# Optimization experiments

Measured on AMD Instinct MI355X. Metric: run time of the kernel, lower is better.

## Reference

```python
import jax, jax.numpy as jnp
import numpy as np

B, S, E, H = 4, 2048, 1024, 4
D = E // H  # head_dim = 256


def setup_inputs() -> dict:
    key = jax.random.key(0)
    ks = jax.random.split(key, 9)
    scale = 1.0 / np.sqrt(E)
    return {
        "hidden_states": jax.random.normal(ks[0], (B, S, E), jnp.float32),
        "Wq": jax.random.normal(ks[1], (E, E), jnp.float32) * scale,
        "Wk": jax.random.normal(ks[2], (E, E), jnp.float32) * scale,
        "Wv": jax.random.normal(ks[3], (E, E), jnp.float32) * scale,
        "Wo": jax.random.normal(ks[4], (E, E), jnp.float32) * scale,
        "bo": jax.random.normal(ks[5], (E,), jnp.float32) * 0.02,
        "betas": jax.random.normal(ks[6], (1, H, 1, 1), jnp.float32),
        "mem": jax.random.uniform(ks[7], (H, D, D), jnp.float32),
        "z": jax.random.uniform(ks[8], (H, D, 1), jnp.float32),
    }


def _split_heads(t):  # [B,S,E] -> [B,H,S,D]
    return t.reshape(B, S, H, D).transpose(0, 2, 1, 3)


def reference(hidden_states, Wq, Wk, Wv, Wo, bo, betas, mem, z):
    q = _split_heads(hidden_states @ Wq)  # [B,H,S,D]
    k = _split_heads(hidden_states @ Wk)
    v = _split_heads(hidden_states @ Wv)

    # linear-attention feature map (ELU + 1)
    sigma_q = jax.nn.elu(q) + 1.0
    sigma_k = jax.nn.elu(k) + 1.0

    # compressive-memory read: mem [H,D,D], z [H,D,1] broadcast over batch
    A_mem = (sigma_q @ mem) / (sigma_q @ z + 1e-6)  # [B,H,S,D]

    # standard causal softmax attention
    attn_weights = jnp.einsum("bhqd,bhkd->bhqk", q, k)
    causal = jnp.tril(jnp.ones((S, S), bool))
    mask_value = jnp.finfo(attn_weights.dtype).min
    attn_weights = jnp.where(causal, attn_weights, mask_value)
    attn_weights = jax.nn.softmax(attn_weights, axis=-1)
    attn_output = jnp.einsum("bhqk,bhkd->bhqd", attn_weights, v)

    # per-head sigmoid gate mixing memory read and local attention
    gate = jax.nn.sigmoid(betas)  # [1,H,1,1]
    attn_output = gate * A_mem + (1.0 - gate) * attn_output

    # memory update (delta rule)
    delta = (sigma_k @ mem) / (sigma_k @ z + 1e-6)  # [B,H,S,D]
    mem_new = mem + jnp.einsum("bhsd,bhse->bhde", sigma_k, v - delta)  # [B,H,D,D]
    z_new = z + sigma_k.sum(axis=-2, keepdims=True).transpose(0, 1, 3, 2)  # [B,H,D,1]

    out = attn_output.transpose(0, 2, 1, 3).reshape(B, S, E) @ Wo + bo
    return out, mem_new, z_new
```

## Files before the change

### kernel.cpp

```cpp
#include <hip/hip_runtime.h>
#include <math.h>

#define Bn 4
#define Sn 2048
#define En 1024
#define Hn 4
#define Dn 256

typedef _Float16 half8 __attribute__((ext_vector_type(8)));
typedef _Float16 half4v __attribute__((ext_vector_type(4)));
typedef float floatx4 __attribute__((ext_vector_type(4)));

#define MFMA16(a, b, c) __builtin_amdgcn_mfma_f32_16x16x32_f16((a), (b), (c), 0, 0, 0)

__device__ __forceinline__ float elup1(float x) {
    return x > 0.0f ? x + 1.0f : __expf(x);
}

__global__ void cvt_h_k(const float* __restrict__ src, _Float16* __restrict__ dst, int n4) {
    int idx = blockIdx.x * 256 + threadIdx.x;
    const int stride = gridDim.x * 256;
    for (; idx < n4; idx += stride) {
        float4 v = ((const float4*)src)[idx];
        half4v o;
        o[0] = (_Float16)v.x; o[1] = (_Float16)v.y;
        o[2] = (_Float16)v.z; o[3] = (_Float16)v.w;
        ((half4v*)dst)[idx] = o;
    }
}

__global__ __launch_bounds__(256) void trans_f32f16_k(
    const float* __restrict__ src, _Float16* __restrict__ dst, int R, int C) {
    __shared__ float T[64][65];
    const int tid = threadIdx.x;
    const int c0 = blockIdx.x * 64, r0 = blockIdx.y * 64;
    src += (size_t)blockIdx.z * R * C;
    dst += (size_t)blockIdx.z * R * C;
    {
        const int tr = tid >> 2, tc = (tid & 3) * 16;
        const float* s = src + (size_t)(r0 + tr) * C + c0 + tc;
        #pragma unroll
        for (int i = 0; i < 4; ++i) {
            float4 v = *(const float4*)(s + i * 4);
            T[tr][tc + i * 4 + 0] = v.x;
            T[tr][tc + i * 4 + 1] = v.y;
            T[tr][tc + i * 4 + 2] = v.z;
            T[tr][tc + i * 4 + 3] = v.w;
        }
    }
    __syncthreads();
    {
        const int cr = tid >> 2, rc = (tid & 3) * 16;
        half8 h0, h1;
        #pragma unroll
        for (int i = 0; i < 8; ++i) h0[i] = (_Float16)T[rc + i][cr];
        #pragma unroll
        for (int i = 0; i < 8; ++i) h1[i] = (_Float16)T[rc + 8 + i][cr];
        _Float16* d = dst + (size_t)(c0 + cr) * R + r0 + rc;
        *(half8*)d = h0;
        *(half8*)(d + 8) = h1;
    }
}

__global__ __launch_bounds__(256) void trans_h16_k(
    const _Float16* __restrict__ Vh, _Float16* __restrict__ Vtg) {
    __shared__ __align__(16) unsigned short T[64 * 72];
    const int tid = threadIdx.x;
    const int s0 = blockIdx.x * 64;
    const int e0 = blockIdx.y * 64;
    const int b = blockIdx.z;
    const int h = e0 >> 8, d0 = e0 & 255;
    {
        const int tr = tid >> 2, tc = (tid & 3) * 16;
        const _Float16* s = Vh + (size_t)(b * Sn + s0 + tr) * En + e0 + tc;
        _Float16* d = (_Float16*)T + tr * 72 + tc;
        *(half8*)d = *(const half8*)s;
        *(half8*)(d + 8) = *(const half8*)(s + 8);
    }
    __syncthreads();
    {
        const int dr = tid >> 2, sc = (tid & 3) * 16;
        const _Float16* Tp = (const _Float16*)T;
        half8 h0, h1;
        #pragma unroll
        for (int i = 0; i < 8; ++i) h0[i] = Tp[(sc + i) * 72 + dr];
        #pragma unroll
        for (int i = 0; i < 8; ++i) h1[i] = Tp[(sc + 8 + i) * 72 + dr];
        _Float16* d = Vtg + (size_t)((b * 4 + h) * 256 + d0 + dr) * (size_t)Sn + s0 + sc;
        *(half8*)d = h0;
        *(half8*)(d + 8) = h1;
    }
}

template <bool OUT32>
__global__ __launch_bounds__(256) void gemm_fused_k(
    const _Float16* __restrict__ A, const _Float16* __restrict__ Bt,
    _Float16* __restrict__ Qo, _Float16* __restrict__ Ko, _Float16* __restrict__ Vo,
    float* __restrict__ C32, const float* __restrict__ bias) {
    __shared__ __align__(16) unsigned short Ah[128 * 72];
    __shared__ __align__(16) unsigned short Bh[128 * 72];
    const int tid = threadIdx.x;
    const int lane = tid & 63, w = tid >> 6, quad = lane >> 4, l15 = lane & 15;
    const int bm = blockIdx.y * 128, bn = blockIdx.x * 128;
    const int wr = (w >> 1) * 64, wc = (w & 1) * 64;
    floatx4 acc[4][4];
    #pragma unroll
    for (int mt = 0; mt < 4; ++mt)
        #pragma unroll
        for (int nt = 0; nt < 4; ++nt) acc[mt][nt] = (floatx4){0.f, 0.f, 0.f, 0.f};

    const int srow = tid >> 1, skoff = (tid & 1) * 32;
    const _Float16* as = A + (size_t)(bm + srow) * 1024 + skoff;
    const _Float16* bs = Bt + (size_t)(bn + srow) * 1024 + skoff;
    _Float16* ad = (_Float16*)Ah + srow * 72 + skoff;
    _Float16* bd = (_Float16*)Bh + srow * 72 + skoff;
    const _Float16* AhF = (const _Float16*)Ah;
    const _Float16* BhF = (const _Float16*)Bh;

    for (int k0 = 0; k0 < 1024; k0 += 64) {
        if (k0) __syncthreads();
        #pragma unroll
        for (int u = 0; u < 4; ++u) {
            *(half8*)(ad + u * 8) = *(const half8*)(as + k0 + u * 8);
            *(half8*)(bd + u * 8) = *(const half8*)(bs + k0 + u * 8);
        }
        __syncthreads();
        #pragma unroll
        for (int ks = 0; ks < 2; ++ks) {
            half8 af[4], bf[4];
            #pragma unroll
            for (int mt = 0; mt < 4; ++mt)
                af[mt] = *(const half8*)(AhF + (wr + mt * 16 + l15) * 72 + ks * 32 + quad * 8);
            #pragma unroll
            for (int nt = 0; nt < 4; ++nt)
                bf[nt] = *(const half8*)(BhF + (wc + nt * 16 + l15) * 72 + ks * 32 + quad * 8);
            #pragma unroll
            for (int mt = 0; mt < 4; ++mt)
                #pragma unroll
                for (int nt = 0; nt < 4; ++nt)
                    acc[mt][nt] = MFMA16(af[mt], bf[nt], acc[mt][nt]);
        }
    }
    #pragma unroll
    for (int mt = 0; mt < 4; ++mt)
        #pragma unroll
        for (int nt = 0; nt < 4; ++nt)
            #pragma unroll
            for (int r = 0; r < 4; ++r) {
                const int row = bm + wr + mt * 16 + quad * 4 + r;
                const int col = bn + wc + nt * 16 + l15;
                if constexpr (OUT32) {
                    C32[(size_t)row * 1024 + col] = acc[mt][nt][r] + bias[col];
                } else {
                    const int m = col >> 10, c = col & 1023;
                    _Float16* dst = (m == 0) ? Qo : ((m == 1) ? Ko : Vo);
                    dst[(size_t)row * 1024 + c] = (_Float16)acc[mt][nt][r];
                }
            }
}

__global__ __launch_bounds__(256, 3) void flash_gate_k(
    const _Float16* __restrict__ Qh, const _Float16* __restrict__ Khg,
    const _Float16* __restrict__ Vtg, const _Float16* __restrict__ memT,
    const float* __restrict__ zp, const float* __restrict__ betas,
    _Float16* __restrict__ Cmb, _Float16* __restrict__ Opart,
    float* __restrict__ mpart, float* __restrict__ lpart) {
    __shared__ __align__(16) unsigned short Pb[4 * 16 * 40];
    const int tid = threadIdx.x;
    const int lane = tid & 63;
    const int w = tid >> 6, quad = lane >> 4, l15 = lane & 15;
    const int bx = blockIdx.x, bh = blockIdx.y;
    const int b = bh >> 2, h = bh & 3;

    int qt, kt0, kt1, unit;
    if (bx < 32) {
        qt = 31 - (bx >> 1);
        unit = bx & 1;
        kt0 = unit ? (qt + 1) : 0;
        kt1 = unit ? (2 * qt + 2) : (qt + 1);
    } else {
        qt = 15 - (bx - 32);
        unit = 0;
        kt0 = 0;
        kt1 = 2 * qt + 2;
    }
    const bool two = (bx < 32);
    const int q0 = qt * 64;

    const _Float16* Qrow = Qh + (size_t)(b * Sn + q0 + w * 16 + l15) * En + h * Dn;
    half8 qf[8];
    #pragma unroll
    for (int kc = 0; kc < 8; ++kc) qf[kc] = *(const half8*)(Qrow + kc * 32 + quad * 8);

    floatx4 acc[17];
    #pragma unroll
    for (int nt = 0; nt < 17; ++nt) acc[nt] = (floatx4){0.f, 0.f, 0.f, 0.f};
    half8 ones;
    #pragma unroll
    for (int j = 0; j < 8; ++j) ones[j] = (_Float16)1.0f;

    const float gate = 1.0f / (1.0f + __expf(-betas[h]));
    const float omg = 1.0f - gate;
    _Float16* Cb = Cmb + (size_t)(b * Sn + q0 + w * 16) * En + h * Dn;
    _Float16* PbF = (_Float16*)Pb;

    if (unit == 0) {
        float denp = 0.0f;
        const _Float16* memh = memT + (size_t)h * Dn * Dn + (size_t)l15 * Dn + quad * 8;
        for (int dc = 0; dc < 8; ++dc) {
            half8 sv;
            const float* zb = zp + h * Dn + dc * 32 + quad * 8;
            #pragma unroll
            for (int j = 0; j < 8; ++j) {
                const float s = elup1((float)qf[dc][j]);
                sv[j] = (_Float16)s;
                denp += s * zb[j];
            }
            #pragma unroll
            for (int nt = 0; nt < 16; ++nt) {
                half8 bmf = *(const half8*)(memh + (size_t)(nt * 16) * Dn + dc * 32);
                acc[nt] = MFMA16(sv, bmf, acc[nt]);
            }
        }
        denp += __shfl_xor(denp, 16);
        denp += __shfl_xor(denp, 32);
        const float deninv = 1.0f / (denp + 1e-6f);
        float den4[4];
        #pragma unroll
        for (int r = 0; r < 4; ++r) den4[r] = __shfl(deninv, quad * 4 + r);
        #pragma unroll
        for (int nt = 0; nt < 16; ++nt)
            #pragma unroll
            for (int r = 0; r < 4; ++r) {
                Cb[(size_t)(quad * 4 + r) * En + nt * 16 + l15] =
                    (_Float16)(gate * acc[nt][r] * den4[r]);
                acc[nt][r] = 0.0f;
            }
    }

    const _Float16* kb0 = Khg + (size_t)(b * Sn + kt0 * 32 + l15) * En + h * Dn + quad * 8;
    const _Float16* kb1 = kb0 + (size_t)16 * En;
    const _Float16* vb = Vtg + (size_t)(bh * 256 + l15) * Sn + kt0 * 32 + quad * 8;
    float mold[4] = {-1e30f, -1e30f, -1e30f, -1e30f};

    for (int kt = kt0; kt < kt1; ++kt) {
        floatx4 S0 = (floatx4){0.f, 0.f, 0.f, 0.f};
        floatx4 S1 = (floatx4){0.f, 0.f, 0.f, 0.f};
        #pragma unroll
        for (int kc = 0; kc < 8; ++kc) {
            half8 kf0 = *(const half8*)(kb0 + kc * 32);
            half8 kf1 = *(const half8*)(kb1 + kc * 32);
            S0 = MFMA16(qf[kc], kf0, S0);
            S1 = MFMA16(qf[kc], kf1, S1);
        }
        kb0 += (size_t)32 * En;
        kb1 += (size_t)32 * En;
        if (kt >= 2 * qt) {
            const int k0 = kt * 32;
            #pragma unroll
            for (int r = 0; r < 4; ++r) {
                const int qg = q0 + w * 16 + quad * 4 + r;
                if (k0 + l15 > qg) S0[r] = -1e30f;
                if (k0 + 16 + l15 > qg) S1[r] = -1e30f;
            }
        }
        float alpha[4];
        bool nr = true;
        #pragma unroll
        for (int r = 0; r < 4; ++r) {
            float mx = fmaxf(S0[r], S1[r]);
            mx = fmaxf(mx, __shfl_xor(mx, 1));
            mx = fmaxf(mx, __shfl_xor(mx, 2));
            mx = fmaxf(mx, __shfl_xor(mx, 4));
            mx = fmaxf(mx, __shfl_xor(mx, 8));
            const float mnew = fmaxf(mold[r], mx);
            alpha[r] = __expf(mold[r] - mnew);
            nr = nr && (mnew == mold[r]);
            mold[r] = mnew;
            const float p0 = __expf(S0[r] - mnew);
            const float p1 = __expf(S1[r] - mnew);
            _Float16* pr = PbF + (w * 16 + quad * 4 + r) * 40;
            pr[l15] = (_Float16)p0;
            pr[16 + l15] = (_Float16)p1;
        }
        if (__ballot(nr) != 0xFFFFFFFFFFFFFFFFull) {
            #pragma unroll
            for (int nt = 0; nt < 17; ++nt) {
                acc[nt][0] *= alpha[0];
                acc[nt][1] *= alpha[1];
                acc[nt][2] *= alpha[2];
                acc[nt][3] *= alpha[3];
            }
        }
        __asm__ volatile("s_waitcnt lgkmcnt(0)" ::: "memory");
        half8 pf = *(const half8*)(PbF + (w * 16 + l15) * 40 + quad * 8);
        #pragma unroll
        for (int nt = 0; nt < 16; ++nt) {
            half8 vf = *(const half8*)(vb + (size_t)(nt * 16) * Sn);
            acc[nt] = MFMA16(pf, vf, acc[nt]);
        }
        acc[16] = MFMA16(pf, ones, acc[16]);
        vb += 32;
    }

    if (!two) {
        #pragma unroll
        for (int r = 0; r < 4; ++r) {
            const float sc = omg / acc[16][r];
            #pragma unroll
            for (int nt = 0; nt < 16; ++nt) {
                const size_t idx = (size_t)(quad * 4 + r) * En + nt * 16 + l15;
                Cb[idx] = (_Float16)((float)Cb[idx] + acc[nt][r] * sc);
            }
        }
    } else {
        const int pidx = ((qt - 16) * 16 + bh) * 2 + unit;
        _Float16* Op = Opart + ((size_t)pidx * 64 + w * 16) * 256;
        #pragma unroll
        for (int nt = 0; nt < 16; ++nt)
            #pragma unroll
            for (int r = 0; r < 4; ++r)
                Op[(quad * 4 + r) * 256 + nt * 16 + l15] = (_Float16)acc[nt][r];
        if (l15 == 0) {
            #pragma unroll
            for (int r = 0; r < 4; ++r) {
                mpart[pidx * 64 + w * 16 + quad * 4 + r] = mold[r];
                lpart[pidx * 64 + w * 16 + quad * 4 + r] = acc[16][r];
            }
        }
    }
}

__global__ __launch_bounds__(256) void merge_k(
    const _Float16* __restrict__ Opart, const float* __restrict__ mpart,
    const float* __restrict__ lpart, const float* __restrict__ betas,
    _Float16* __restrict__ Cmb) {
    const int qi = blockIdx.x;
    const int bh = blockIdx.y;
    const int b = bh >> 2, h = bh & 3;
    const int tid = threadIdx.x;
    const int idx = (qi * 16 + bh) * 2;
    const float gate = 1.0f / (1.0f + __expf(-betas[h]));
    const float omg = 1.0f - gate;
    const int rsub = tid >> 6;
    const int c0 = (tid & 63) * 4;
    const _Float16* O0 = Opart + (size_t)idx * 64 * 256;
    const _Float16* O1 = O0 + 64 * 256;
    const int q0 = (16 + qi) * 64;
    for (int chunk = 0; chunk < 16; ++chunk) {
        const int r = chunk * 4 + rsub;
        const float m0 = mpart[idx * 64 + r], l0 = lpart[idx * 64 + r];
        const float m1 = mpart[(idx + 1) * 64 + r], l1 = lpart[(idx + 1) * 64 + r];
        const float mm = fmaxf(m0, m1);
        const float s0 = __expf(m0 - mm), s1 = __expf(m1 - mm);
        const float rl = omg / (l0 * s0 + l1 * s1);
        half4v o0 = *(const half4v*)(O0 + r * 256 + c0);
        half4v o1 = *(const half4v*)(O1 + r * 256 + c0);
        _Float16* cp = Cmb + (size_t)(b * Sn + q0 + r) * En + h * Dn + c0;
        half4v cv = *(half4v*)cp;
        #pragma unroll
        for (int j = 0; j < 4; ++j)
            cv[j] = (_Float16)((float)cv[j] + ((float)o0[j] * s0 + (float)o1[j] * s1) * rl);
        *(half4v*)cp = cv;
    }
}

__global__ __launch_bounds__(256) void delta_ut_k(
    const _Float16* __restrict__ Kg, _Float16* __restrict__ Vtg,
    _Float16* __restrict__ SkT, const _Float16* __restrict__ memT,
    const float* __restrict__ zp) {
    __shared__ __align__(16) unsigned short L[256 * 72];
    const int tid = threadIdx.x;
    const int lane = tid & 63;
    const int w = tid >> 6, quad = lane >> 4, l15 = lane & 15;
    const int s0 = blockIdx.x * 64;
    const int bh = blockIdx.y;
    const int b = bh >> 2, h = bh & 3;
    _Float16* Lf = (_Float16*)L;

    const _Float16* Krow = Kg + (size_t)(b * Sn + s0 + w * 16 + l15) * En + h * Dn;
    half8 skf[8];
    float denp = 0.0f;
    #pragma unroll
    for (int kc = 0; kc < 8; ++kc) {
        half8 kv = *(const half8*)(Krow + kc * 32 + quad * 8);
        const float* zb = zp + h * Dn + kc * 32 + quad * 8;
        #pragma unroll
        for (int j = 0; j < 8; ++j) {
            const float s = elup1((float)kv[j]);
            skf[kc][j] = (_Float16)s;
            denp += s * zb[j];
        }
    }
    denp += __shfl_xor(denp, 16);
    denp += __shfl_xor(denp, 32);
    const float deninv = 1.0f / (denp + 1e-6f);
    float den4[4];
    #pragma unroll
    for (int r = 0; r < 4; ++r) den4[r] = __shfl(deninv, quad * 4 + r);

    floatx4 acc[16];
    #pragma unroll
    for (int nt = 0; nt < 16; ++nt) acc[nt] = (floatx4){0.f, 0.f, 0.f, 0.f};
    const _Float16* memh = memT + (size_t)h * Dn * Dn + (size_t)l15 * Dn + quad * 8;
    #pragma unroll
    for (int kc = 0; kc < 8; ++kc)
        #pragma unroll
        for (int nt = 0; nt < 16; ++nt) {
            half8 bmf = *(const half8*)(memh + (size_t)(nt * 16) * Dn + kc * 32);
            acc[nt] = MFMA16(skf[kc], bmf, acc[nt]);
        }

    #pragma unroll
    for (int nt = 0; nt < 16; ++nt)
        #pragma unroll
        for (int r = 0; r < 4; ++r)
            Lf[(nt * 16 + l15) * 72 + w * 16 + quad * 4 + r] =
                (_Float16)(acc[nt][r] * den4[r]);
    __syncthreads();
    {
        _Float16* Vrow = Vtg + (size_t)(bh * 256 + tid) * Sn + s0;
        #pragma unroll
        for (int u = 0; u < 8; ++u) {
            half8 v = *(const half8*)(Vrow + u * 8);
            half8 d = *(const half8*)(Lf + tid * 72 + u * 8);
            #pragma unroll
            for (int j = 0; j < 8; ++j) v[j] = v[j] - d[j];
            *(half8*)(Vrow + u * 8) = v;
        }
    }
    __syncthreads();
    #pragma unroll
    for (int kc = 0; kc < 8; ++kc)
        #pragma unroll
        for (int j = 0; j < 8; ++j)
            Lf[(kc * 32 + quad * 8 + j) * 72 + w * 16 + l15] = skf[kc][j];
    __syncthreads();
    {
        _Float16* Srow = SkT + (size_t)(bh * 256 + tid) * Sn + s0;
        #pragma unroll
        for (int u = 0; u < 8; ++u)
            *(half8*)(Srow + u * 8) = *(const half8*)(Lf + tid * 72 + u * 8);
    }
}

__global__ __launch_bounds__(256) void memupd_k(
    const _Float16* __restrict__ SkT, const _Float16* __restrict__ UT,
    const float* __restrict__ memp, float* __restrict__ mem_new) {
    __shared__ __align__(16) unsigned short Ah[64 * 72];
    __shared__ __align__(16) unsigned short Bh[64 * 72];
    const int tid = threadIdx.x;
    const int lane = tid & 63, w = tid >> 6, quad = lane >> 4, l15 = lane & 15;
    const int bn = blockIdx.x * 64, bm = blockIdx.y * 64;
    const int bh = blockIdx.z, h = bh & 3;
    const _Float16* Ab = SkT + (size_t)(bh * 256 + bm) * Sn;
    const _Float16* Bb = UT + (size_t)(bh * 256 + bn) * Sn;
    floatx4 acc[4];
    #pragma unroll
    for (int nt = 0; nt < 4; ++nt) acc[nt] = (floatx4){0.f, 0.f, 0.f, 0.f};

    const int srow = tid >> 2, skoff = (tid & 3) * 16;
    _Float16* ad = (_Float16*)Ah + srow * 72 + skoff;
    _Float16* bd = (_Float16*)Bh + srow * 72 + skoff;
    const _Float16* AhF = (const _Float16*)Ah;
    const _Float16* BhF = (const _Float16*)Bh;

    for (int k0 = 0; k0 < Sn; k0 += 64) {
        if (k0) __syncthreads();
        *(half8*)ad = *(const half8*)(Ab + (size_t)srow * Sn + k0 + skoff);
        *(half8*)(ad + 8) = *(const half8*)(Ab + (size_t)srow * Sn + k0 + skoff + 8);
        *(half8*)bd = *(const half8*)(Bb + (size_t)srow * Sn + k0 + skoff);
        *(half8*)(bd + 8) = *(const half8*)(Bb + (size_t)srow * Sn + k0 + skoff + 8);
        __syncthreads();
        #pragma unroll
        for (int ks = 0; ks < 2; ++ks) {
            half8 af = *(const half8*)(AhF + (w * 16 + l15) * 72 + ks * 32 + quad * 8);
            #pragma unroll
            for (int nt = 0; nt < 4; ++nt) {
                half8 bf = *(const half8*)(BhF + (nt * 16 + l15) * 72 + ks * 32 + quad * 8);
                acc[nt] = MFMA16(af, bf, acc[nt]);
            }
        }
    }
    const float* mh = memp + (size_t)h * Dn * Dn;
    float* mo = mem_new + (size_t)bh * Dn * Dn;
    #pragma unroll
    for (int nt = 0; nt < 4; ++nt)
        #pragma unroll
        for (int r = 0; r < 4; ++r) {
            const int d = bm + w * 16 + quad * 4 + r;
            const int e = bn + nt * 16 + l15;
            mo[(size_t)d * Dn + e] = mh[(size_t)d * Dn + e] + acc[nt][r];
        }
}

__global__ __launch_bounds__(256) void znew_init_k(
    const float* __restrict__ zp, float* __restrict__ z_new) {
    const int bh = blockIdx.x;
    const int h = bh & 3;
    z_new[(size_t)bh * Dn + threadIdx.x] = zp[(size_t)h * Dn + threadIdx.x];
}

__global__ __launch_bounds__(256) void znew_acc_k(
    const _Float16* __restrict__ Kg, float* __restrict__ z_new) {
    const int bh = blockIdx.y;
    const int b = bh >> 2;
    const int h = bh & 3;
    const int s0 = blockIdx.x * 256;
    const _Float16* Kb = Kg + (size_t)(b * Sn + s0) * En + h * Dn;
    float acc = 0.0f;
    for (int s = 0; s < 256; ++s) acc += elup1((float)Kb[(size_t)s * En + threadIdx.x]);
    atomicAdd(&z_new[(size_t)bh * Dn + threadIdx.x], acc);
}

extern "C" void kernel_launch(void* const* d_in, const int* in_sizes, int n_in,
                              void* d_out, int out_size, void* d_ws, size_t ws_size,
                              hipStream_t stream) {
    const float* hidden = (const float*)d_in[0];
    const float* Wq = (const float*)d_in[1];
    const float* Wk = (const float*)d_in[2];
    const float* Wv = (const float*)d_in[3];
    const float* Wo = (const float*)d_in[4];
    const float* bo = (const float*)d_in[5];
    const float* betas = (const float*)d_in[6];
    const float* memp = (const float*)d_in[7];
    const float* zp = (const float*)d_in[8];

    float* out = (float*)d_out;
    float* mem_new = out + (size_t)Bn * Sn * En;
    float* z_new = mem_new + (size_t)Bn * Hn * Dn * Dn;

    const size_t BSE = (size_t)Bn * Sn * En;
    _Float16* p = (_Float16*)d_ws;
    _Float16* Qh = p;    p += BSE;
    _Float16* Kh = p;    p += BSE;
    _Float16* Vh = p;    p += BSE;
    _Float16* Vtg = p;   p += BSE;
    _Float16* Cmb = p;   p += BSE;
    _Float16* Opart = p; p += BSE;
    _Float16* hh = p;    p += BSE;
    _Float16* WqT = p;   p += (size_t)3 * En * En;
    _Float16* WoT = p;   p += (size_t)En * En;
    _Float16* memT = p;  p += (size_t)Hn * Dn * Dn;
    float* fp = (float*)p;
    float* mpart = fp;   fp += 512 * 64;
    float* lpart = fp;   fp += 512 * 64;
    _Float16* SkT = hh;

    trans_f32f16_k<<<dim3(16, 16, 1), 256, 0, stream>>>(Wq, WqT, En, En);
    trans_f32f16_k<<<dim3(16, 16, 1), 256, 0, stream>>>(Wk, WqT + (size_t)En * En, En, En);
    trans_f32f16_k<<<dim3(16, 16, 1), 256, 0, stream>>>(Wv, WqT + (size_t)2 * En * En, En, En);
    trans_f32f16_k<<<dim3(16, 16, 1), 256, 0, stream>>>(Wo, WoT, En, En);
    trans_f32f16_k<<<dim3(4, 4, 4), 256, 0, stream>>>(memp, memT, Dn, Dn);
    cvt_h_k<<<2048, 256, 0, stream>>>(hidden, hh, (int)(BSE / 4));

    gemm_fused_k<false><<<dim3(24, 64), 256, 0, stream>>>(
        hh, WqT, Qh, Kh, Vh, nullptr, nullptr);

    trans_h16_k<<<dim3(32, 16, 4), 256, 0, stream>>>(Vh, Vtg);

    flash_gate_k<<<dim3(48, 16), 256, 0, stream>>>(
        Qh, Kh, Vtg, memT, zp, betas, Cmb, Opart, mpart, lpart);
    merge_k<<<dim3(16, 16), 256, 0, stream>>>(Opart, mpart, lpart, betas, Cmb);

    delta_ut_k<<<dim3(32, 16), 256, 0, stream>>>(Kh, Vtg, SkT, memT, zp);
    memupd_k<<<dim3(4, 4, 16), 256, 0, stream>>>(SkT, Vtg, memp, mem_new);

    znew_init_k<<<16, 256, 0, stream>>>(zp, z_new);
    znew_acc_k<<<dim3(8, 16), 256, 0, stream>>>(Kh, z_new);

    gemm_fused_k<true><<<dim3(8, 64), 256, 0, stream>>>(
        Cmb, WoT, nullptr, nullptr, nullptr, out, bo);
}
```

Baseline: 711.4 us.

## Stage K and V tiles in shared memory with register prefetch

Before, each of the four waves loaded its own K and V fragments straight from global memory every key tile. Now the block loads each 32-key tile of K and V^T once, cooperatively, into LDS, and the next tile is prefetched into registers while the current one is used. This removes four-fold redundant global/L2 traffic per block and hides load latency. The cost is two __syncthreads per iteration, more registers for the prefetch buffers, and about 37KB of extra LDS, which may limit occupancy under launch_bounds(256,3).

Measured after the change: 645.1 us. 1.1x faster.

```diff
diff --git a/kernel.cpp b/kernel.cpp
--- a/kernel.cpp
+++ b/kernel.cpp
@@ -165,7 +165,10 @@
     const float* __restrict__ zp, const float* __restrict__ betas,
     _Float16* __restrict__ Cmb, _Float16* __restrict__ Opart,
     float* __restrict__ mpart, float* __restrict__ lpart) {
-    __shared__ __align__(16) unsigned short Pb[4 * 16 * 40];
+    __shared__ __align__(16) unsigned short Ksh[32 * 260];
+    __shared__ __align__(16) unsigned short Vs[4 * 256 * 8];
+    __shared__ __align__(16) unsigned short Pb[64 * 40];
+
     const int tid = threadIdx.x;
     const int lane = tid & 63;
     const int w = tid >> 6, quad = lane >> 4, l15 = lane & 15;
@@ -202,6 +205,8 @@
     const float gate = 1.0f / (1.0f + __expf(-betas[h]));
     const float omg = 1.0f - gate;
     _Float16* Cb = Cmb + (size_t)(b * Sn + q0 + w * 16) * En + h * Dn;
+    _Float16* KshF = (_Float16*)Ksh;
+    _Float16* VsF = (_Float16*)Vs;
     _Float16* PbF = (_Float16*)Pb;
 
     if (unit == 0) {
@@ -238,25 +243,48 @@
             }
     }
 
-    const _Float16* kb0 = Khg + (size_t)(b * Sn + kt0 * 32 + l15) * En + h * Dn + quad * 8;
-    const _Float16* kb1 = kb0 + (size_t)16 * En;
-    const _Float16* vb = Vtg + (size_t)(bh * 256 + l15) * Sn + kt0 * 32 + quad * 8;
+    const _Float16* Kbase = Khg + (size_t)(b * Sn) * En + h * Dn;
+    const _Float16* Vtb = Vtg + (size_t)bh * 256 * (size_t)Sn;
+    const _Float16* kptr = Kbase + (size_t)(kt0 * 32 + (tid >> 3)) * En + (tid & 7) * 32;
+    const _Float16* vptr = Vtb + (size_t)tid * Sn + kt0 * 32;
+    half8 kr[4], vr[4];
+    #pragma unroll
+    for (int u = 0; u < 4; ++u) {
+        kr[u] = *(const half8*)(kptr + u * 8);
+        vr[u] = *(const half8*)(vptr + u * 8);
+    }
+    const int kwoff = (tid >> 3) * 260 + (tid & 7) * 32;
     float mold[4] = {-1e30f, -1e30f, -1e30f, -1e30f};
 
     for (int kt = kt0; kt < kt1; ++kt) {
+        const int k0 = kt * 32;
+        __syncthreads();
+        #pragma unroll
+        for (int u = 0; u < 4; ++u) {
+            *(half8*)(KshF + kwoff + u * 8) = kr[u];
+            *(half8*)(VsF + (u * 256 + tid) * 8) = vr[u];
+        }
+        __syncthreads();
+        if (kt + 1 < kt1) {
+            kptr += (size_t)32 * En;
+            vptr += 32;
+            #pragma unroll
+            for (int u = 0; u < 4; ++u) {
+                kr[u] = *(const half8*)(kptr + u * 8);
+                vr[u] = *(const half8*)(vptr + u * 8);
+            }
+        }
+
         floatx4 S0 = (floatx4){0.f, 0.f, 0.f, 0.f};
         floatx4 S1 = (floatx4){0.f, 0.f, 0.f, 0.f};
         #pragma unroll
         for (int kc = 0; kc < 8; ++kc) {
-            half8 kf0 = *(const half8*)(kb0 + kc * 32);
-            half8 kf1 = *(const half8*)(kb1 + kc * 32);
+            half8 kf0 = *(const half8*)(KshF + l15 * 260 + kc * 32 + quad * 8);
+            half8 kf1 = *(const half8*)(KshF + (16 + l15) * 260 + kc * 32 + quad * 8);
             S0 = MFMA16(qf[kc], kf0, S0);
             S1 = MFMA16(qf[kc], kf1, S1);
         }
-        kb0 += (size_t)32 * En;
-        kb1 += (size_t)32 * En;
         if (kt >= 2 * qt) {
-            const int k0 = kt * 32;
             #pragma unroll
             for (int r = 0; r < 4; ++r) {
                 const int qg = q0 + w * 16 + quad * 4 + r;
@@ -296,11 +324,10 @@
         half8 pf = *(const half8*)(PbF + (w * 16 + l15) * 40 + quad * 8);
         #pragma unroll
         for (int nt = 0; nt < 16; ++nt) {
-            half8 vf = *(const half8*)(vb + (size_t)(nt * 16) * Sn);
+            half8 vf = *(const half8*)(VsF + (quad * 256 + nt * 16 + l15) * 8);
             acc[nt] = MFMA16(pf, vf, acc[nt]);
         }
         acc[16] = MFMA16(pf, ones, acc[16]);
-        vb += 32;
     }
 
     if (!two) {
```
